# Performance work log

Hardware: AMD Instinct MI355X
Metric: run time of the kernel (lower is better)

The kernel has to match this reference:

```python
import jax, jax.numpy as jnp
import numpy as np

H = 2880
NH = 64        # query heads
NKV = 8        # kv heads
DH = 64        # head dim
GROUP = NH // NKV
THETA = 150000.0
FACTOR = 32.0
SCALE = 1.0 / np.sqrt(DH)
INIT_STD = 0.02
SINK_INIT = 4.0


def setup_inputs() -> dict:
    key = jax.random.key(0)
    ks = jax.random.split(key, 6)
    B, T = 2, 1024
    x = jax.random.normal(ks[0], (B, T, H), dtype=jnp.float32)
    positions = jnp.tile(jnp.arange(T, dtype=jnp.int32), (B, 1))
    causal_mask = jnp.tril(jnp.ones((T, T), dtype=bool))
    Wq = INIT_STD * jax.random.normal(ks[1], (H, NH * DH), dtype=jnp.float32)
    Wk = INIT_STD * jax.random.normal(ks[2], (H, NKV * DH), dtype=jnp.float32)
    Wv = INIT_STD * jax.random.normal(ks[3], (H, NKV * DH), dtype=jnp.float32)
    Wo = INIT_STD * jax.random.normal(ks[4], (NH * DH, H), dtype=jnp.float32)
    bq = jnp.zeros((NH * DH,), jnp.float32)
    bk = jnp.zeros((NKV * DH,), jnp.float32)
    bv = jnp.zeros((NKV * DH,), jnp.float32)
    bo = jnp.zeros((H,), jnp.float32)
    sink_logit = jnp.full((NH,), SINK_INIT, dtype=jnp.float32)
    return {
        'x': x, 'positions': positions, 'causal_mask': causal_mask,
        'Wq': Wq, 'bq': bq, 'Wk': Wk, 'bk': bk, 'Wv': Wv, 'bv': bv,
        'Wo': Wo, 'bo': bo, 'sink_logit': sink_logit,
        'is_sliding_layer': 1, 'sliding_window': 128,
    }


def _rope(x, pos):
    # x: [B, h, T, DH], pos: [B, T] ints. YaRN-style stretched positions: pos/FACTOR.
    inv_freq = 1.0 / (THETA ** (jnp.arange(0, DH, 2, dtype=jnp.float32) / DH))  # [DH/2]
    freqs = (pos.astype(jnp.float32) / FACTOR)[:, :, None] * inv_freq           # [B, T, DH/2]
    cos = jnp.cos(freqs)[:, None].astype(x.dtype)  # [B, 1, T, DH/2]
    sin = jnp.sin(freqs)[:, None].astype(x.dtype)
    x1, x2 = x[..., 0::2], x[..., 1::2]
    r1 = x1 * cos - x2 * sin
    r2 = x1 * sin + x2 * cos
    return jnp.stack([r1, r2], axis=-1).reshape(x.shape)  # re-interleave even/odd


def reference(x, positions, causal_mask, Wq, bq, Wk, bk, Wv, bv, Wo, bo,
              sink_logit, is_sliding_layer, sliding_window):
    B, T, _ = x.shape
    q = (x @ Wq + bq).reshape(B, T, NH, DH).transpose(0, 2, 1, 3)   # [B,NH,T,DH]
    k = (x @ Wk + bk).reshape(B, T, NKV, DH)
    v = (x @ Wv + bv).reshape(B, T, NKV, DH)
    # GQA expand: each kv head repeated GROUP times contiguously (head h -> kv h//GROUP)
    k = jnp.repeat(k, GROUP, axis=2).transpose(0, 2, 1, 3)          # [B,NH,T,DH]
    v = jnp.repeat(v, GROUP, axis=2).transpose(0, 2, 1, 3)
    q = _rope(q, positions)
    k = _rope(k, positions)
    att = jnp.einsum('bhtd,bhsd->bhts', q, k) * SCALE               # [B,NH,T,T]
    mask = causal_mask
    if is_sliding_layer:
        i = jnp.arange(T)
        dist = i[:, None] - i[None, :]
        mask = mask & (dist >= 0) & (dist < sliding_window)
    att = jnp.where(mask[None, None], att, jnp.asarray(-1e30, att.dtype))
    # learned per-head sink logit appended as an extra softmax column
    sink = jnp.broadcast_to(sink_logit.reshape(1, NH, 1, 1).astype(att.dtype), (B, NH, T, 1))
    att = jnp.concatenate([att, sink], axis=-1)                     # [B,NH,T,T+1]
    p = jax.nn.softmax(att, axis=-1)[..., :-1]                      # drop sink column
    y = jnp.einsum('bhts,bhsd->bhtd', p, v)
    y = y.transpose(0, 2, 1, 3).reshape(B, T, NH * DH)
    return y @ Wo + bo
```

## Files before the change

kernel.cpp:

```cpp
#include <hip/hip_runtime.h>

typedef unsigned short u16;
typedef __attribute__((ext_vector_type(8))) short bf16x8;
typedef __attribute__((ext_vector_type(4))) float f32x4;

#define MFMA16(a,b,c) __builtin_amdgcn_mfma_f32_16x16x32_bf16((a),(b),(c),0,0,0)

__device__ __forceinline__ float b2f(u16 u){
  unsigned v = ((unsigned)u) << 16; float f;
  __builtin_memcpy(&f, &v, 4); return f;
}
__device__ __forceinline__ u16 f2b(float f){
  unsigned v; __builtin_memcpy(&v, &f, 4);
  v += 0x7FFFu + ((v >> 16) & 1u);
  return (u16)(v >> 16);
}
__device__ __forceinline__ float scrub(float v, float lim){
  return fminf(fmaxf(v, -lim), lim);
}
__device__ __forceinline__ void gload16(const void* g, void* l){
  __builtin_amdgcn_global_load_lds(
      (const __attribute__((address_space(1))) unsigned int*)g,
      (__attribute__((address_space(3))) unsigned int*)l, 16, 0, 0);
}

__device__ __forceinline__ void cvtT_tile(float (*tile)[33],
    u16* __restrict__ dst, const float* __restrict__ src,
    int rows, int cols, int bx, int by, int tid){
  int n0 = bx * 32, r0 = by * 32;
  int tx = tid & 31, ty = tid >> 5;
#pragma unroll
  for (int i = 0; i < 4; i++)
    tile[ty + i * 8][tx] = src[(size_t)(r0 + ty + i * 8) * cols + n0 + tx];
  __syncthreads();
#pragma unroll
  for (int i = 0; i < 4; i++)
    dst[(size_t)(n0 + ty + i * 8) * rows + r0 + tx] = f2b(tile[tx][ty + i * 8]);
}

__global__ __launch_bounds__(256) void k_prep1(
    u16* __restrict__ xb, const float* __restrict__ x,
    u16* __restrict__ wqT, const float* __restrict__ Wq){
  __shared__ float tile[32][33];
  int b = blockIdx.x, tid = threadIdx.x;
  if (b < 5760){
    int i = b * 256 + tid;
    float4 v = ((const float4*)x)[i];
    u16 o[4] = { f2b(v.x), f2b(v.y), f2b(v.z), f2b(v.w) };
    *(uint2*)&xb[(size_t)i * 4] = *(const uint2*)o;
    return;
  }
  b -= 5760;
  cvtT_tile(tile, wqT, Wq, 2880, 4096, b % 128, b / 128, tid);
}

__global__ __launch_bounds__(256) void k_prep2(
    u16* __restrict__ wkvT, const float* __restrict__ Wk,
    const float* __restrict__ Wv){
  __shared__ float tile[32][33];
  int b = blockIdx.x, tid = threadIdx.x;
  if (b < 1440){ cvtT_tile(tile, wkvT, Wk, 2880, 512, b % 16, b / 16, tid); return; }
  b -= 1440;
  cvtT_tile(tile, wkvT + (size_t)512 * 2880, Wv, 2880, 512, b % 16, b / 16, tid);
}

__global__ __launch_bounds__(256) void k_prep3(
    u16* __restrict__ woT, const float* __restrict__ Wo){
  __shared__ float tile[32][33];
  int b = blockIdx.x, tid = threadIdx.x;
  cvtT_tile(tile, woT, Wo, 4096, 2880, b % 90, b / 90, tid);
}

template<int BN, int F32OUT, int ROPE>
__global__ __launch_bounds__(512, 1) void k_gx(
    const u16* __restrict__ A, const u16* __restrict__ BT, const u16* __restrict__ BT2,
    const float* __restrict__ b0, const float* __restrict__ b1, const float* __restrict__ b2,
    void* __restrict__ C, const int* __restrict__ pos, int M, int N, int K, int ldc){
  constexpr int NF   = BN / 32;
  constexpr int FULL = (BN - 32) / 64;
  constexpr int BUFE = 16384 + BN * 64;
  constexpr int VMW  = 4 + FULL;
  __shared__ u16 lds[3][BUFE];

  const int tid = threadIdx.x;
  const int w = tid >> 6, l = tid & 63;
  const int wm = w >> 1, wn = w & 1;
  const int lr = l & 15, lh = l >> 4;
  const int bid = blockIdx.x;
  const int mt = bid & 7, nt = bid >> 3;
  const int m0 = mt << 8, n0 = nt * BN;

  const int srow = tid >> 3;
  const int skc  = (tid & 7) << 3;
  const int ssw  = (srow & 7) << 3;
  const int rsw  = (lr & 7) << 3;
  const int rrow = tid >> 3;

  f32x4 acc[4][NF];
#pragma unroll
  for (int mm = 0; mm < 4; mm++)
#pragma unroll
    for (int nn = 0; nn < NF; nn++){ acc[mm][nn][0]=0.f; acc[mm][nn][1]=0.f; acc[mm][nn][2]=0.f; acc[mm][nn][3]=0.f; }

#define STAGE_A(b, kt, c) \
  gload16(&A[(size_t)(m0 + (c)*64 + srow) * K + (kt) + (skc ^ ssw)], \
          (void*)&lds[b][((c)*64 + srow) * 64 + skc])
#define STAGE_BF(b, kt, c) { \
  int _r = n0 + (c)*64 + srow; \
  const u16* _bt = BT; if (ROPE && _r >= 4096){ _bt = BT2; _r -= 4096; } \
  gload16(&_bt[(size_t)_r * K + (kt) + (skc ^ ssw)], \
          (void*)&lds[b][16384 + ((c)*64 + srow) * 64 + skc]); }
#define STAGE_BR(b, kt) if (tid < 256){ \
  int _r = n0 + FULL*64 + rrow; \
  const u16* _bt = BT; if (ROPE && _r >= 4096){ _bt = BT2; _r -= 4096; } \
  gload16(&_bt[(size_t)_r * K + (kt) + (skc ^ ((rrow & 7) << 3))], \
          (void*)&lds[b][16384 + (FULL*64 + rrow) * 64 + skc]); }

#define RD_A(dst, b, mm, kk) dst = *(const bf16x8*)&lds[b][((wm<<6) + ((mm)<<4) + lr) * 64 + ((((kk)<<5) + (lh<<3)) ^ rsw)]
#define RD_B(dst, b, nn, kk) dst = *(const bf16x8*)&lds[b][16384 + (wn*(BN/2) + (nn)*16 + lr) * 64 + ((((kk)<<5) + (lh<<3)) ^ rsw)]

  const int NT = K >> 6;
#pragma unroll
  for (int tt = 0; tt < 2; ++tt){
    int kt = tt << 6;
#pragma unroll
    for (int c = 0; c < 4; ++c) STAGE_A(tt, kt, c);
#pragma unroll
    for (int c = 0; c < FULL; ++c) STAGE_BF(tt, kt, c);
    STAGE_BR(tt, kt);
  }
  asm volatile("s_waitcnt vmcnt(%0)" :: "i"(VMW) : "memory");
  __builtin_amdgcn_s_barrier();

  int cb = 0;
  for (int t = 0; t < NT; ++t){
    int sb = cb + 2; if (sb >= 3) sb -= 3;
    const int kt2 = (t + 2) << 6;
    const bool ds = (t + 2) < NT;

    bf16x8 bf[NF][2];
#pragma unroll
    for (int nn = 0; nn < NF; nn++){ RD_B(bf[nn][0], cb, nn, 0); RD_B(bf[nn][1], cb, nn, 1); }

#pragma unroll
    for (int mm = 0; mm < 4; mm++){
      bf16x8 a0, a1;
      RD_A(a0, cb, mm, 0); RD_A(a1, cb, mm, 1);
      if (ds){
        STAGE_A(sb, kt2, mm);
        if (mm < FULL) STAGE_BF(sb, kt2, mm);
        if (mm == 2) STAGE_BR(sb, kt2);
      }
      __builtin_amdgcn_s_setprio(1);
#pragma unroll
      for (int nn = 0; nn < NF; nn++) acc[mm][nn] = MFMA16(a0, bf[nn][0], acc[mm][nn]);
#pragma unroll
      for (int nn = 0; nn < NF; nn++) acc[mm][nn] = MFMA16(a1, bf[nn][1], acc[mm][nn]);
      __builtin_amdgcn_s_setprio(0);
    }

    if (ds) asm volatile("s_waitcnt vmcnt(%0)" :: "i"(VMW) : "memory");
    else    asm volatile("s_waitcnt vmcnt(0)" ::: "memory");
    __builtin_amdgcn_s_barrier();
    cb += 1; if (cb >= 3) cb -= 3;
  }

#pragma unroll
  for (int mm = 0; mm < 4; mm++){
    int grow = m0 + (wm << 6) + (mm << 4) + (lh << 2);
#pragma unroll
    for (int nn = 0; nn < NF; nn++){
      int gcol = n0 + wn * (BN / 2) + nn * 16 + lr;
      float bs;
      if (ROPE) bs = (gcol < 4096) ? b0[gcol] : ((gcol < 4608) ? b1[gcol - 4096] : b2[gcol - 4608]);
      else      bs = b0[gcol];
      if (ROPE && gcol < 4608){
        int ii = (gcol & 63) >> 1;
        float inv = exp2f(-0.53733146f * (float)ii);
        float sgn = (lr & 1) ? 1.f : -1.f;
#pragma unroll
        for (int r = 0; r < 4; r++){
          float v = acc[mm][nn][r] + bs;
          float ang = (float)pos[grow + r] * 0.03125f * inv;
          float s, c; __sincosf(ang, &s, &c);
          float p = __shfl_xor(v, 1);
          v = v * c + p * sgn * s;
          ((u16*)C)[(size_t)(grow + r) * ldc + gcol] = f2b(scrub(v, 1e9f));
        }
      } else {
#pragma unroll
        for (int r = 0; r < 4; r++){
          float v = scrub(acc[mm][nn][r] + bs, 1e9f);
          size_t off = (size_t)(grow + r) * ldc + gcol;
          if (F32OUT) ((float*)C)[off] = v;
          else        ((u16*)C)[off]   = f2b(v);
        }
      }
    }
  }
#undef STAGE_A
#undef STAGE_BF
#undef STAGE_BR
#undef RD_A
#undef RD_B
}

__global__ __launch_bounds__(256) void k_attn(
    const u16* __restrict__ qkv, const float* __restrict__ sink,
    u16* __restrict__ y, const int* __restrict__ slide_p,
    const int* __restrict__ win_p){
  __shared__ u16 Ks[64][72];
  __shared__ u16 VTs[64][72];
  __shared__ u16 Plds[4][32][72];

  int bid = blockIdx.x;
  int qt = bid & 7, h = (bid >> 3) & 63, b = bid >> 9;
  int t0 = qt << 7;
  int g = h >> 3;
  int kcol = 4096 + g * 64, vcol = 4608 + g * 64;
  int tid = threadIdx.x, w = tid >> 6, l = tid & 63;
  int lr = l & 15, lh = l >> 4;
  int win = (*slide_p) ? (*win_p) : (1 << 30);
  int tq0 = t0 + w * 32;

  bf16x8 qf[2][2];
#pragma unroll
  for (int m = 0; m < 2; m++)
#pragma unroll
    for (int kk = 0; kk < 2; kk++){
      int q = tq0 + m * 16 + lr;
      qf[m][kk] = *(const bf16x8*)&qkv[(size_t)(b * 1024 + q) * 5120 + h * 64 + kk * 32 + lh * 8];
    }

  float run_max[2] = {-1e30f, -1e30f};
  float run_sum[2] = {0.f, 0.f};
  f32x4 acc_o[4][2];
#pragma unroll
  for (int dt = 0; dt < 4; dt++)
#pragma unroll
    for (int m = 0; m < 2; m++){ acc_o[dt][m][0]=0.f; acc_o[dt][m][1]=0.f; acc_o[dt][m][2]=0.f; acc_o[dt][m][3]=0.f; }

  for (int c = 0; c < 4; c++){
    int key0 = t0 - 128 + c * 64;
#pragma unroll
    for (int it = 0; it < 2; ++it){
      int idx = it * 256 + tid;
      int key = idx >> 3, dd = (idx & 7) << 3;
      int gk = key0 + key;
      uint4 kq = make_uint4(0, 0, 0, 0);
      uint4 vq = make_uint4(0, 0, 0, 0);
      if (gk >= 0){
        size_t rb = (size_t)(b * 1024 + gk) * 5120;
        kq = *(const uint4*)&qkv[rb + kcol + dd];
        vq = *(const uint4*)&qkv[rb + vcol + dd];
      }
      *(uint4*)&Ks[key][dd] = kq;
      const u16* tv = (const u16*)&vq;
#pragma unroll
      for (int j = 0; j < 8; j++) VTs[dd + j][key] = tv[j];
    }
    __syncthreads();

    bool rel = (key0 + 63 >= tq0 - (win - 1)) && (key0 <= tq0 + 31);
    if (rel){
      f32x4 sacc[2][4];
#pragma unroll
      for (int m = 0; m < 2; m++)
#pragma unroll
        for (int n = 0; n < 4; n++){ sacc[m][n][0]=0.f; sacc[m][n][1]=0.f; sacc[m][n][2]=0.f; sacc[m][n][3]=0.f; }
#pragma unroll
      for (int kk = 0; kk < 2; kk++){
#pragma unroll
        for (int n = 0; n < 4; n++){
          bf16x8 kf = *(const bf16x8*)&Ks[n * 16 + lr][kk * 32 + lh * 8];
          sacc[0][n] = MFMA16(kf, qf[0][kk], sacc[0][n]);
          sacc[1][n] = MFMA16(kf, qf[1][kk], sacc[1][n]);
        }
      }
#pragma unroll
      for (int m = 0; m < 2; m++){
        int qrow = tq0 + m * 16 + lr;
        float cmax = -INFINITY;
#pragma unroll
        for (int n = 0; n < 4; n++)
#pragma unroll
          for (int r = 0; r < 4; r++){
            int key = key0 + n * 16 + lh * 4 + r;
            float s = scrub(sacc[m][n][r] * 0.125f, 1e30f);
            bool valid = (key >= 0) && (key <= qrow) && (qrow - key < win);
            s = valid ? s : -INFINITY;
            sacc[m][n][r] = s;
            cmax = fmaxf(cmax, s);
          }
        cmax = fmaxf(cmax, __shfl_xor(cmax, 16));
        cmax = fmaxf(cmax, __shfl_xor(cmax, 32));
        float mnew = fmaxf(run_max[m], cmax);
        float corr = __expf(run_max[m] - mnew);
        run_max[m] = mnew;
        float rsum = 0.f;
#pragma unroll
        for (int n = 0; n < 4; n++)
#pragma unroll
          for (int r = 0; r < 4; r++){
            float p = __expf(sacc[m][n][r] - mnew);
            sacc[m][n][r] = p;
            rsum += p;
          }
        rsum += __shfl_xor(rsum, 16);
        rsum += __shfl_xor(rsum, 32);
        run_sum[m] = run_sum[m] * corr + rsum;
#pragma unroll
        for (int dt = 0; dt < 4; dt++) acc_o[dt][m] *= corr;
#pragma unroll
        for (int n = 0; n < 4; n++)
#pragma unroll
          for (int r = 0; r < 4; r++)
            Plds[w][m * 16 + lr][n * 16 + lh * 4 + r] = f2b(sacc[m][n][r]);
      }
#pragma unroll
      for (int ks = 0; ks < 2; ks++){
        bf16x8 pb[2];
#pragma unroll
        for (int m = 0; m < 2; m++)
          pb[m] = *(const bf16x8*)&Plds[w][m * 16 + lr][ks * 32 + lh * 8];
#pragma unroll
        for (int dt = 0; dt < 4; dt++){
          bf16x8 vf = *(const bf16x8*)&VTs[dt * 16 + lr][ks * 32 + lh * 8];
          acc_o[dt][0] = MFMA16(vf, pb[0], acc_o[dt][0]);
          acc_o[dt][1] = MFMA16(vf, pb[1], acc_o[dt][1]);
        }
      }
    }
    __syncthreads();
  }

  float sk = sink[h];
  float osc[2];
#pragma unroll
  for (int m = 0; m < 2; m++){
    float Mf = fmaxf(run_max[m], sk);
    float t = __expf(run_max[m] - Mf);
    float denom = run_sum[m] * t + __expf(sk - Mf);
    osc[m] = t / denom;
  }
#pragma unroll
  for (int dt = 0; dt < 4; dt++)
#pragma unroll
    for (int m = 0; m < 2; m++)
#pragma unroll
      for (int r = 0; r < 4; r++){
        int d = dt * 16 + lh * 4 + r;
        int q = tq0 + m * 16 + lr;
        y[(size_t)(b * 1024 + q) * 4096 + h * 64 + d] = f2b(scrub(acc_o[dt][m][r] * osc[m], 1e9f));
      }
}

extern "C" void kernel_launch(void* const* d_in, const int* in_sizes, int n_in,
                              void* d_out, int out_size, void* d_ws, size_t ws_size,
                              hipStream_t stream){
  const float* x    = (const float*)d_in[0];
  const int*   pos  = (const int*)d_in[1];
  const float* Wq   = (const float*)d_in[3];
  const float* bq   = (const float*)d_in[4];
  const float* Wk   = (const float*)d_in[5];
  const float* bk   = (const float*)d_in[6];
  const float* Wv   = (const float*)d_in[7];
  const float* bv   = (const float*)d_in[8];
  const float* Wo   = (const float*)d_in[9];
  const float* bo   = (const float*)d_in[10];
  const float* sink = (const float*)d_in[11];
  const int* slide  = (const int*)d_in[12];
  const int* winp   = (const int*)d_in[13];
  float* out = (float*)d_out;

  char* ws = (char*)d_ws;
  u16* xb   = (u16*)(ws + 0);
  u16* ybuf = (u16*)(ws + 0);
  u16* wkvT = (u16*)(ws + 11796480);
  u16* qkv  = (u16*)(ws + 17694720);
  u16* wqT  = (u16*)(ws + 38666240);
  u16* woT  = (u16*)(ws + 38666240);

  k_prep1<<<5760 + 11520, 256, 0, stream>>>(xb, x, wqT, Wq);
  k_prep2<<<1440 + 1440, 256, 0, stream>>>(wkvT, Wk, Wv);
  k_gx<160, 0, 1><<<256, 512, 0, stream>>>(xb, wqT, wkvT, bq, bk, bv, qkv, pos, 2048, 5120, 2880, 5120);
  k_prep3<<<11520, 256, 0, stream>>>(woT, Wo);
  k_attn<<<1024, 256, 0, stream>>>(qkv, sink, ybuf, slide, winp);
  k_gx<96, 1, 0><<<240, 512, 0, stream>>>(ybuf, woT, woT, bo, bo, bo, out, pos, 2048, 2880, 4096, 2880);
}
```

Baseline: 182.0 us.

## Fuse prep kernels into neighbours and reorder GEMM tile rasterization

Merges the Wk/Wv transpose-convert into the first prep kernel and folds the Wo transpose-convert into the attention kernel as extra blocks sharing a unified shared-memory buffer, cutting launches from six to four and letting the Wo conversion overlap attention. It also changes the GEMM block-to-tile mapping so consecutive blocks walk along N within one M tile rather than along M, altering L2 reuse of A versus B. Attention blocks and conversion blocks now compete for the same CUs, and the new rasterization may reduce reuse of the weight tiles.

```diff
diff --git a/kernel.cpp b/kernel.cpp
--- a/kernel.cpp
+++ b/kernel.cpp
@@ -40,7 +40,9 @@
 
 __global__ __launch_bounds__(256) void k_prep1(
     u16* __restrict__ xb, const float* __restrict__ x,
-    u16* __restrict__ wqT, const float* __restrict__ Wq){
+    u16* __restrict__ wqT, const float* __restrict__ Wq,
+    u16* __restrict__ wkvT, const float* __restrict__ Wk,
+    const float* __restrict__ Wv){
   __shared__ float tile[32][33];
   int b = blockIdx.x, tid = threadIdx.x;
   if (b < 5760){
@@ -51,27 +53,14 @@
     return;
   }
   b -= 5760;
-  cvtT_tile(tile, wqT, Wq, 2880, 4096, b % 128, b / 128, tid);
-}
-
-__global__ __launch_bounds__(256) void k_prep2(
-    u16* __restrict__ wkvT, const float* __restrict__ Wk,
-    const float* __restrict__ Wv){
-  __shared__ float tile[32][33];
-  int b = blockIdx.x, tid = threadIdx.x;
+  if (b < 11520){ cvtT_tile(tile, wqT, Wq, 2880, 4096, b % 128, b / 128, tid); return; }
+  b -= 11520;
   if (b < 1440){ cvtT_tile(tile, wkvT, Wk, 2880, 512, b % 16, b / 16, tid); return; }
   b -= 1440;
   cvtT_tile(tile, wkvT + (size_t)512 * 2880, Wv, 2880, 512, b % 16, b / 16, tid);
 }
 
-__global__ __launch_bounds__(256) void k_prep3(
-    u16* __restrict__ woT, const float* __restrict__ Wo){
-  __shared__ float tile[32][33];
-  int b = blockIdx.x, tid = threadIdx.x;
-  cvtT_tile(tile, woT, Wo, 4096, 2880, b % 90, b / 90, tid);
-}
-
-template<int BN, int F32OUT, int ROPE>
+template<int BN, int NTC, int F32OUT, int ROPE>
 __global__ __launch_bounds__(512, 1) void k_gx(
     const u16* __restrict__ A, const u16* __restrict__ BT, const u16* __restrict__ BT2,
     const float* __restrict__ b0, const float* __restrict__ b1, const float* __restrict__ b2,
@@ -87,7 +76,7 @@
   const int wm = w >> 1, wn = w & 1;
   const int lr = l & 15, lh = l >> 4;
   const int bid = blockIdx.x;
-  const int mt = bid & 7, nt = bid >> 3;
+  const int mt = bid / NTC, nt = bid % NTC;
   const int m0 = mt << 8, n0 = nt * BN;
 
   const int srow = tid >> 3;
@@ -205,13 +194,23 @@
 #undef RD_B
 }
 
-__global__ __launch_bounds__(256) void k_attn(
+__global__ __launch_bounds__(256) void k_attn_prep(
     const u16* __restrict__ qkv, const float* __restrict__ sink,
     u16* __restrict__ y, const int* __restrict__ slide_p,
-    const int* __restrict__ win_p){
-  __shared__ u16 Ks[64][72];
-  __shared__ u16 VTs[64][72];
-  __shared__ u16 Plds[4][32][72];
+    const int* __restrict__ win_p,
+    u16* __restrict__ woT, const float* __restrict__ Wo){
+  __shared__ char smem[36864];
+
+  if (blockIdx.x >= 1024){
+    int b = blockIdx.x - 1024;
+    float (*tile)[33] = (float(*)[33])smem;
+    cvtT_tile(tile, woT, Wo, 4096, 2880, b % 90, b / 90, threadIdx.x);
+    return;
+  }
+
+  u16 (*Ks)[72]       = (u16(*)[72])smem;
+  u16 (*VTs)[72]      = (u16(*)[72])(smem + 9216);
+  u16 (*Plds)[32][72] = (u16(*)[32][72])(smem + 18432);
 
   int bid = blockIdx.x;
   int qt = bid & 7, h = (bid >> 3) & 63, b = bid >> 9;
@@ -381,10 +380,8 @@
   u16* wqT  = (u16*)(ws + 38666240);
   u16* woT  = (u16*)(ws + 38666240);
 
-  k_prep1<<<5760 + 11520, 256, 0, stream>>>(xb, x, wqT, Wq);
-  k_prep2<<<1440 + 1440, 256, 0, stream>>>(wkvT, Wk, Wv);
-  k_gx<160, 0, 1><<<256, 512, 0, stream>>>(xb, wqT, wkvT, bq, bk, bv, qkv, pos, 2048, 5120, 2880, 5120);
-  k_prep3<<<11520, 256, 0, stream>>>(woT, Wo);
-  k_attn<<<1024, 256, 0, stream>>>(qkv, sink, ybuf, slide, winp);
-  k_gx<96, 1, 0><<<240, 512, 0, stream>>>(ybuf, woT, woT, bo, bo, bo, out, pos, 2048, 2880, 4096, 2880);
-}
+  k_prep1<<<5760 + 11520 + 2880, 256, 0, stream>>>(xb, x, wqT, Wq, wkvT, Wk, Wv);
+  k_gx<160, 32, 0, 1><<<256, 512, 0, stream>>>(xb, wqT, wkvT, bq, bk, bv, qkv, pos, 2048, 5120, 2880, 5120);
+  k_attn_prep<<<1024 + 11520, 256, 0, stream>>>(qkv, sink, ybuf, slide, winp, woT, Wo);
+  k_gx<96, 30, 1, 0><<<240, 512, 0, stream>>>(ybuf, woT, woT, bo, bo, bo, out, pos, 2048, 2880, 4096, 2880);
+}
```

Measured after the change: 173.5 us, median of 2. 1.05x faster.
